# Kernel optimization log

Measured on AMD Instinct MI355X. Metric: run time of the kernel, lower is better.

## Reference

```python
import jax, jax.numpy as jnp
import numpy as np

V, E, H, T = 50000, 128, 256, 9
H2 = H // 2
B, S = 128, 512


def setup_inputs() -> dict:
    key = jax.random.key(0)
    ks = jax.random.split(key, 12)
    sc = 0.05
    return {
        "x": jax.random.randint(ks[0], (B, S), 0, V, dtype=jnp.int64) if False else jax.random.randint(ks[0], (B, S), 0, V).astype(jnp.int64),
        "mask": jnp.ones((B, S), dtype=jnp.int32),
        "embed": jax.random.normal(ks[1], (V, E), jnp.float32) * sc,
        "W_ih_f": jax.random.normal(ks[2], (4 * H2, E), jnp.float32) * sc,
        "W_hh_f": jax.random.normal(ks[3], (4 * H2, H2), jnp.float32) * sc,
        "b_f": jax.random.normal(ks[4], (4 * H2,), jnp.float32) * sc,
        "W_ih_b": jax.random.normal(ks[5], (4 * H2, E), jnp.float32) * sc,
        "W_hh_b": jax.random.normal(ks[6], (4 * H2, H2), jnp.float32) * sc,
        "b_b": jax.random.normal(ks[7], (4 * H2,), jnp.float32) * sc,
        "W_out": jax.random.normal(ks[8], (T, H), jnp.float32) * sc,
        "b_out": jax.random.normal(ks[9], (T,), jnp.float32) * sc,
        "start_trans": jax.random.normal(ks[10], (T,), jnp.float32) * sc,
        "trans": jax.random.normal(ks[11], (T, T), jnp.float32) * sc,
        "end_trans": jax.random.normal(jax.random.fold_in(key, 99), (T,), jnp.float32) * sc,
    }


def _lstm_dir(xg, W_hh, reverse):
    # xg: [B,S,4*H2] precomputed input projections (+bias)
    if reverse:
        xg = xg[:, ::-1]
    b = xg.shape[0]
    h0 = jnp.zeros((b, H2), xg.dtype)

    def step(carry, xt):
        h, c = carry
        g = xt + h @ W_hh.T
        i, f, gg, o = jnp.split(g, 4, axis=-1)
        c = jax.nn.sigmoid(f) * c + jax.nn.sigmoid(i) * jnp.tanh(gg)
        h = jax.nn.sigmoid(o) * jnp.tanh(c)
        return (h, c), h

    _, hs = jax.lax.scan(step, (h0, h0), jnp.swapaxes(xg, 0, 1))
    hs = jnp.swapaxes(hs, 0, 1)  # [B,S,H2]
    if reverse:
        hs = hs[:, ::-1]
    return hs


def _emissions(x, embed, W_ih_f, W_hh_f, b_f, W_ih_b, W_hh_b, b_b, W_out, b_out):
    emb = embed[x]  # [B,S,E]
    xg_f = jnp.einsum('bse,ge->bsg', emb, W_ih_f) + b_f
    xg_b = jnp.einsum('bse,ge->bsg', emb, W_ih_b) + b_b
    h_f = _lstm_dir(xg_f, W_hh_f, False)
    h_b = _lstm_dir(xg_b, W_hh_b, True)
    feats = jnp.concatenate([h_f, h_b], axis=-1)  # [B,S,H]
    return jnp.einsum('bsh,th->bst', feats, W_out) + b_out  # [B,S,T]


def _viterbi(emissions, mask, start_trans, trans, end_trans):
    # emissions [B,S,T], mask [B,S] (1 = valid prefix)
    m = mask.astype(bool)
    score0 = start_trans + emissions[:, 0]  # [B,T]

    def fwd_step(score, inp):
        em_t, m_t = inp  # [B,T], [B]
        nxt = score[:, :, None] + trans[None] + em_t[:, None, :]  # [B,prev,next]
        best = nxt.max(axis=1)
        idx = nxt.argmax(axis=1).astype(jnp.int32)  # [B,T] backpointers
        score = jnp.where(m_t[:, None], best, score)
        return score, idx

    em_rest = jnp.swapaxes(emissions[:, 1:], 0, 1)  # [S-1,B,T]
    m_rest = jnp.swapaxes(m[:, 1:], 0, 1)  # [S-1,B]
    score, history = jax.lax.scan(fwd_step, score0, (em_rest, m_rest))
    final = score + end_trans
    best_scores = final.max(axis=-1)  # [B]
    cur = final.argmax(axis=-1).astype(jnp.int32)  # [B] tag at last valid step

    def back_step(cur, inp):
        hist_t, m_t = inp  # [B,T], [B]
        tag = jnp.where(m_t, cur, -1)  # -1 pads positions beyond seq end
        prev = jnp.take_along_axis(hist_t, cur[:, None], axis=1)[:, 0]
        cur = jnp.where(m_t, prev, cur)
        return cur, tag

    cur0, tags_rev = jax.lax.scan(back_step, cur, (history[::-1], m_rest[::-1]))
    paths = jnp.concatenate(
        [cur0[:, None], jnp.swapaxes(tags_rev, 0, 1)[:, ::-1]], axis=1)  # [B,S]
    return paths, best_scores


def reference(x, mask, embed, W_ih_f, W_hh_f, b_f, W_ih_b, W_hh_b, b_b,
              W_out, b_out, start_trans, trans, end_trans):
    emissions = _emissions(x, embed, W_ih_f, W_hh_f, b_f,
                           W_ih_b, W_hh_b, b_b, W_out, b_out)
    paths, best_scores = _viterbi(emissions, mask, start_trans, trans, end_trans)
    return paths, best_scores
```

## Files before the change

kernel.cpp:

```cpp
#include <hip/hip_runtime.h>
#include <stdint.h>

#define S_LEN 512
#define NT 9

typedef __attribute__((ext_vector_type(8)))  short          bf16x8;
typedef __attribute__((ext_vector_type(4)))  float          f32x4;
typedef __attribute__((ext_vector_type(16))) unsigned short u16x16;
typedef __attribute__((ext_vector_type(4)))  unsigned int   u32x4;

static __device__ __forceinline__ unsigned short f2bf(float f) {
    union { float f; unsigned u; } c; c.f = f;
    return (unsigned short)((c.u + 0x7fffu + ((c.u >> 16) & 1u)) >> 16);
}
static __device__ __forceinline__ float bf2f(unsigned short h) {
    union { unsigned u; float f; } c; c.u = ((unsigned)h) << 16;
    return c.f;
}
static __device__ __forceinline__ bf16x8 cvt8(const float* p) {
    f32x4 a = *(const f32x4*)p, b = *(const f32x4*)(p + 4);
    bf16x8 fr;
    fr[0]=(short)f2bf(a[0]); fr[1]=(short)f2bf(a[1]); fr[2]=(short)f2bf(a[2]); fr[3]=(short)f2bf(a[3]);
    fr[4]=(short)f2bf(b[0]); fr[5]=(short)f2bf(b[1]); fr[6]=(short)f2bf(b[2]); fr[7]=(short)f2bf(b[3]);
    return fr;
}
static __device__ __forceinline__ float sigf(float x) {
    return __builtin_amdgcn_rcpf(1.0f + __expf(-x));
}
static __device__ __forceinline__ float tanhf_(float x) {
    return 1.0f - 2.0f * __builtin_amdgcn_rcpf(1.0f + __expf(2.0f * x));
}
static __device__ __forceinline__ float sel4(f32x4 a, int l4) {
    float x01 = (l4 & 1) ? a[1] : a[0];
    float x23 = (l4 & 1) ? a[3] : a[2];
    return (l4 & 2) ? x23 : x01;
}

static __device__ __forceinline__ void wg_barrier_lds() {
    asm volatile("s_waitcnt lgkmcnt(0)" ::: "memory");
    __builtin_amdgcn_s_barrier();
    asm volatile("" ::: "memory");
}

__global__ __launch_bounds__(512) void k_xg(
    const int* __restrict__ x, const float* __restrict__ embed,
    const float* __restrict__ Wf, const float* __restrict__ bF,
    const float* __restrict__ Wb, const float* __restrict__ bB,
    unsigned short* __restrict__ xg)
{
    const int dir = blockIdx.y, s = blockIdx.x;
    const float* __restrict__ W    = dir ? Wb : Wf;
    const float* __restrict__ bias = dir ? bB : bF;
    const int tid = threadIdx.x;
    const int wv = tid >> 6, L = tid & 63, l15 = L & 15, l4 = L >> 4;

    bf16x8 Bf[4][4];
    float  bq[4];
#pragma unroll
    for (int q = 0; q < 4; ++q) {
        const int gate = q * 128 + wv * 16 + l15;
        bq[q] = bias[gate];
#pragma unroll
        for (int kt = 0; kt < 4; ++kt)
            Bf[q][kt] = cvt8(W + gate * 128 + kt * 32 + l4 * 8);
    }

    __shared__ int tokL[128];
    __shared__ unsigned short stage[2048];

    if (tid < 128) tokL[tid] = x[tid * S_LEN + s];
    const int srow = tid >> 5, scol = tid & 31;
    __syncthreads();

    f32x4 v0 = *(const f32x4*)(embed + (size_t)tokL[srow]      * 128 + scol * 4);
    f32x4 v1 = *(const f32x4*)(embed + (size_t)tokL[16 + srow] * 128 + scol * 4);

    for (int bt16 = 0; bt16 < 8; ++bt16) {
        wg_barrier_lds();
        {
            unsigned short b4[4];
            b4[0]=f2bf(v0[0]); b4[1]=f2bf(v0[1]); b4[2]=f2bf(v0[2]); b4[3]=f2bf(v0[3]);
            int byte = srow * 256 + ((scol * 8) ^ ((srow & 7) << 4));
            *(uint2*)((char*)stage + byte) = *(const uint2*)b4;
        }
        wg_barrier_lds();
        const int nt2 = (bt16 < 6) ? (bt16 + 2) : bt16;
        f32x4 v2 = *(const f32x4*)(embed + (size_t)tokL[nt2 * 16 + srow] * 128 + scol * 4);

        bf16x8 A[4];
#pragma unroll
        for (int kt = 0; kt < 4; ++kt) {
            int byte = l15 * 256 + ((kt * 64 + l4 * 16) ^ ((l15 & 7) << 4));
            A[kt] = *(const bf16x8*)((const char*)stage + byte);
        }
        unsigned short ov[16];
#pragma unroll
        for (int q = 0; q < 4; ++q) {
            f32x4 acc = { bq[q], bq[q], bq[q], bq[q] };
#pragma unroll
            for (int kt = 0; kt < 4; ++kt)
                acc = __builtin_amdgcn_mfma_f32_16x16x32_bf16(A[kt], Bf[q][kt], acc, 0, 0, 0);
            ov[q*4+0]=f2bf(acc[0]); ov[q*4+1]=f2bf(acc[1]);
            ov[q*4+2]=f2bf(acc[2]); ov[q*4+3]=f2bf(acc[3]);
        }
        unsigned short* dst = xg +
            (((((size_t)s * 2 + dir) * 32 + bt16 * 4 + l4) * 8 + wv) * 256 + l15 * 16);
        *(u32x4*)dst       = *(const u32x4*)&ov[0];
        *(u32x4*)(dst + 8) = *(const u32x4*)&ov[8];
        v0 = v1; v1 = v2;
    }
}

__global__ __launch_bounds__(512) void k_lstm(
    const unsigned short* __restrict__ xg,
    const float* __restrict__ Whf, const float* __restrict__ Whb,
    unsigned short* __restrict__ feats)
{
    const int dir = blockIdx.y, bt = blockIdx.x;
    const float* __restrict__ Wh = dir ? Whb : Whf;
    const int tid = threadIdx.x, w = tid >> 6, L = tid & 63, l15 = L & 15, l4 = L >> 4;

    bf16x8 Bf[4][4];
#pragma unroll
    for (int q = 0; q < 4; ++q)
#pragma unroll
        for (int kt = 0; kt < 4; ++kt)
            Bf[q][kt] = cvt8(Wh + (q * 128 + w * 16 + l15) * 128 + kt * 32 + l4 * 8);

    __shared__ unsigned short hl[2048];
    for (int i = tid; i < 1024; i += 512) ((unsigned*)hl)[i] = 0;

    const int ar = l15 & 3;
    int rdoff[4];
#pragma unroll
    for (int kt = 0; kt < 4; ++kt) {
        int p = (kt * 4 + l4 + 2 * ar) & 15;
        rdoff[kt] = ar * 256 + p * 16;
    }
    const int hc = w * 16 + l15;
    const int wroff = l4 * 256 + (((hc >> 3) + 2 * l4) & 15) * 16 + (hc & 7) * 2;

    float c = 0.f;
    const size_t xstep = (size_t)2 * 32 * 8 * 256;
    const size_t xbase = (((size_t)dir * 32 + bt) * 8 + w) * 256 + l15 * 16;
    unsigned short* fptr = feats + ((size_t)(bt * 4 + l4) * 512) * 256 + dir * 128 + hc;

    u16x16 x0 = *(const u16x16*)(xg + xbase + (size_t)(dir ? 511 : 0) * xstep);
    u16x16 x1 = *(const u16x16*)(xg + xbase + (size_t)(dir ? 510 : 1) * xstep);
    __syncthreads();

    for (int t = 0; t < 512; ++t) {
        const char* bufR = (const char*)hl + (t & 1) * 1024;
        char*       bufW = (char*)hl + ((t & 1) ^ 1) * 1024;

        const int tc = (t < 510) ? (t + 2) : t;
        const int s2 = dir ? (511 - tc) : tc;
        u16x16 x2 = *(const u16x16*)(xg + xbase + (size_t)s2 * xstep);

        bf16x8 A[4];
#pragma unroll
        for (int kt = 0; kt < 4; ++kt)
            A[kt] = *(const bf16x8*)(bufR + rdoff[kt]);

        f32x4 acc[4];
#pragma unroll
        for (int q = 0; q < 4; ++q) {
            f32x4 a0 = { bf2f(x0[q*4+0]), bf2f(x0[q*4+1]), bf2f(x0[q*4+2]), bf2f(x0[q*4+3]) };
#pragma unroll
            for (int kt = 0; kt < 4; ++kt)
                a0 = __builtin_amdgcn_mfma_f32_16x16x32_bf16(A[kt], Bf[q][kt], a0, 0, 0, 0);
            acc[q] = a0;
        }
        float ig = sigf(sel4(acc[0], l4));
        float fg = sigf(sel4(acc[1], l4));
        float gg = tanhf_(sel4(acc[2], l4));
        float og = sigf(sel4(acc[3], l4));
        c = fg * c + ig * gg;
        float h = og * tanhf_(c);
        unsigned short hb = f2bf(h);
        *(unsigned short*)(bufW + wroff) = hb;
        const int s_pos = dir ? (511 - t) : t;
        fptr[(size_t)s_pos * 256] = hb;
        wg_barrier_lds();
        x0 = x1; x1 = x2;
    }
}

__global__ __launch_bounds__(256) void k_emis(
    const unsigned short* __restrict__ feats,
    const float* __restrict__ Wout, float* __restrict__ emp)
{
    const int tid = threadIdx.x;
    const int wid = blockIdx.x * 4 + (tid >> 6);
    const int L = tid & 63, l15 = L & 15, l4 = L >> 4;
    const int b = wid >> 5, sg = wid & 31;

    bf16x8 Of[2][4];
#pragma unroll
    for (int d = 0; d < 2; ++d)
#pragma unroll
        for (int kt = 0; kt < 4; ++kt) { bf16x8 z;
#pragma unroll
            for (int i = 0; i < 8; ++i) z[i] = 0; Of[d][kt] = z; }
    if (l15 < NT) {
#pragma unroll
        for (int d = 0; d < 2; ++d)
#pragma unroll
            for (int kt = 0; kt < 4; ++kt)
                Of[d][kt] = cvt8(Wout + l15 * 256 + d * 128 + kt * 32 + l4 * 8);
    }

    const unsigned short* frow = feats + ((size_t)b * 512 + sg * 16 + l15) * 256;
#pragma unroll
    for (int d = 0; d < 2; ++d) {
        bf16x8 A[4];
#pragma unroll
        for (int kt = 0; kt < 4; ++kt)
            A[kt] = *(const bf16x8*)(frow + d * 128 + kt * 32 + l4 * 8);
        f32x4 em0 = {0, 0, 0, 0};
#pragma unroll
        for (int kt = 0; kt < 4; ++kt)
            em0 = __builtin_amdgcn_mfma_f32_16x16x32_bf16(A[kt], Of[d][kt], em0, 0, 0, 0);
        if (l15 < NT) {
#pragma unroll
            for (int j = 0; j < 4; ++j)
                emp[((size_t)(d * 128 + b) * 512 + sg * 16 + l4 * 4 + j) * 9 + l15] = em0[j];
        }
    }
}

__global__ __launch_bounds__(256) void k_viterbi(
    const float* __restrict__ emp, const int* __restrict__ mask,
    const float* __restrict__ bout, const float* __restrict__ startt,
    const float* __restrict__ trans, const float* __restrict__ endt,
    float* __restrict__ out)
{
    const int b = blockIdx.x, tid = threadIdx.x;
    __shared__ float em[512 * 9];
    __shared__ int   msk[512];
    __shared__ unsigned char hist[512 * 9];
    __shared__ unsigned char Gl[32 * 12];
    __shared__ unsigned char bound[32];
    __shared__ int curS;

    const float* pf = emp + (size_t)b * 4608;
    const float* pb = emp + (size_t)(128 + b) * 4608;
    for (int i = tid; i < 4608; i += 256) {
        unsigned q = ((unsigned)i * 7282u) >> 16;
        em[i] = pf[i] + pb[i] + bout[i - 9 * q];
    }
    for (int i = tid; i < 512; i += 256) msk[i] = mask[b * 512 + i];
    __syncthreads();

    if (tid < 64) {
        const int k = (tid < NT) ? tid : 0;
        float trk[9];
#pragma unroll
        for (int j = 0; j < NT; ++j) trk[j] = trans[j * 9 + k];
        float score = startt[k] + em[k];
        for (int t = 1; t < 512; ++t) {
            float v[9];
#pragma unroll
            for (int j = 0; j < NT; ++j) v[j] = __shfl(score, j, 64) + trk[j];
            float m01 = fmaxf(v[0], v[1]), m23 = fmaxf(v[2], v[3]);
            float m45 = fmaxf(v[4], v[5]), m67 = fmaxf(v[6], v[7]);
            float m = fmaxf(fmaxf(fmaxf(m01, m23), fmaxf(m45, m67)), v[8]);
            int bi = 0;
#pragma unroll
            for (int j = 8; j >= 0; --j) if (v[j] == m) bi = j;
            if (msk[t]) score = m + em[t * 9 + k];
            if (tid < NT) hist[t * 9 + tid] = (unsigned char)bi;
        }
        float fin = score + endt[k];
        float bs = -3e38f; int cur = 0;
#pragma unroll
        for (int j = 0; j < NT; ++j) {
            float vv = __shfl(fin, j, 64);
            if (vv > bs) { bs = vv; cur = j; }
        }
        if (tid == 0) { curS = cur; out[65536 + b] = bs; }
    }
    __syncthreads();

    if (tid < 32) {
        const int m = tid;
        int G[9];
#pragma unroll
        for (int k = 0; k < NT; ++k) G[k] = k;
        const int hi = (m == 31) ? 511 : (16 * m + 16);
        for (int t = hi; t >= 16 * m + 1; --t) {
            if (msk[t]) {
#pragma unroll
                for (int k = 0; k < NT; ++k) G[k] = hist[t * 9 + G[k]];
            }
        }
#pragma unroll
        for (int k = 0; k < NT; ++k) Gl[m * 12 + k] = (unsigned char)G[k];
    }
    __syncthreads();

    if (tid == 0) {
        int e = curS;
        bound[31] = (unsigned char)e;
        for (int m = 31; m >= 1; --m) { e = Gl[m * 12 + e]; bound[m - 1] = (unsigned char)e; }
        out[(size_t)b * 512] = (float)Gl[0 * 12 + e];
    }
    __syncthreads();

    if (tid < 32) {
        const int m = tid;
        int ccur = bound[m];
        const int hi = (m == 31) ? 511 : (16 * m + 16);
        for (int t = hi; t >= 16 * m + 1; --t) {
            const int mt = msk[t];
            out[(size_t)b * 512 + t] = (float)(mt ? ccur : -1);
            if (mt) ccur = hist[t * 9 + ccur];
        }
    }
}

extern "C" void kernel_launch(void* const* d_in, const int* in_sizes, int n_in,
                              void* d_out, int out_size, void* d_ws, size_t ws_size,
                              hipStream_t stream) {
    const int*   x      = (const int*)d_in[0];
    const int*   mask   = (const int*)d_in[1];
    const float* embed  = (const float*)d_in[2];
    const float* Wihf   = (const float*)d_in[3];
    const float* Whhf   = (const float*)d_in[4];
    const float* bf_    = (const float*)d_in[5];
    const float* Wihb   = (const float*)d_in[6];
    const float* Whhb   = (const float*)d_in[7];
    const float* bb_    = (const float*)d_in[8];
    const float* Wout   = (const float*)d_in[9];
    const float* bout   = (const float*)d_in[10];
    const float* startt = (const float*)d_in[11];
    const float* trans  = (const float*)d_in[12];
    const float* endt   = (const float*)d_in[13];

    unsigned short* xg    = (unsigned short*)d_ws;
    float*          emp   = (float*)((char*)d_ws + (size_t)134217728);
    unsigned short* feats = (unsigned short*)((char*)d_ws + (size_t)138936320);
    float*          out   = (float*)d_out;

    k_xg     <<<dim3(512, 2), 512, 0, stream>>>(x, embed, Wihf, bf_, Wihb, bb_, xg);
    k_lstm   <<<dim3(32, 2),  512, 0, stream>>>(xg, Whhf, Whhb, feats);
    k_emis   <<<1024,         256, 0, stream>>>(feats, Wout, emp);
    k_viterbi<<<128,          256, 0, stream>>>(emp, mask, bout, startt, trans, endt, out);
}
```

Measured before the change: 462.7 us.

## Repack xg so each LSTM lane loads only its four gate values

The xg projection output is re-laid out so each lane of the recurrent kernel reads just the four gate pre-activations it needs (one u16x4) rather than a 16-element vector. The A-operand row mapping changes (ar = l15>>2) so the useful MFMA output sits in element 0, which removes the per-lane select. The time loop is unrolled by two with a macro, and the feats pointer is advanced incrementally. This cuts global loads and register pressure on the serial critical path, at the cost of narrower, more scattered stores in k_xg.

```diff
diff --git a/kernel.cpp b/kernel.cpp
--- a/kernel.cpp
+++ b/kernel.cpp
@@ -6,7 +6,7 @@
 
 typedef __attribute__((ext_vector_type(8)))  short          bf16x8;
 typedef __attribute__((ext_vector_type(4)))  float          f32x4;
-typedef __attribute__((ext_vector_type(16))) unsigned short u16x16;
+typedef __attribute__((ext_vector_type(4)))  unsigned short u16x4;
 typedef __attribute__((ext_vector_type(4)))  unsigned int   u32x4;
 
 static __device__ __forceinline__ unsigned short f2bf(float f) {
@@ -29,11 +29,6 @@
 }
 static __device__ __forceinline__ float tanhf_(float x) {
     return 1.0f - 2.0f * __builtin_amdgcn_rcpf(1.0f + __expf(2.0f * x));
-}
-static __device__ __forceinline__ float sel4(f32x4 a, int l4) {
-    float x01 = (l4 & 1) ? a[1] : a[0];
-    float x23 = (l4 & 1) ? a[3] : a[2];
-    return (l4 & 2) ? x23 : x01;
 }
 
 static __device__ __forceinline__ void wg_barrier_lds() {
@@ -75,6 +70,8 @@
     f32x4 v0 = *(const f32x4*)(embed + (size_t)tokL[srow]      * 128 + scol * 4);
     f32x4 v1 = *(const f32x4*)(embed + (size_t)tokL[16 + srow] * 128 + scol * 4);
 
+    const int hc = wv * 16 + l15;
+
     for (int bt16 = 0; bt16 < 8; ++bt16) {
         wg_barrier_lds();
         {
@@ -93,20 +90,24 @@
             int byte = l15 * 256 + ((kt * 64 + l4 * 16) ^ ((l15 & 7) << 4));
             A[kt] = *(const bf16x8*)((const char*)stage + byte);
         }
-        unsigned short ov[16];
+        f32x4 acc[4];
 #pragma unroll
         for (int q = 0; q < 4; ++q) {
-            f32x4 acc = { bq[q], bq[q], bq[q], bq[q] };
+            f32x4 a0 = { bq[q], bq[q], bq[q], bq[q] };
 #pragma unroll
             for (int kt = 0; kt < 4; ++kt)
-                acc = __builtin_amdgcn_mfma_f32_16x16x32_bf16(A[kt], Bf[q][kt], acc, 0, 0, 0);
-            ov[q*4+0]=f2bf(acc[0]); ov[q*4+1]=f2bf(acc[1]);
-            ov[q*4+2]=f2bf(acc[2]); ov[q*4+3]=f2bf(acc[3]);
-        }
-        unsigned short* dst = xg +
-            (((((size_t)s * 2 + dir) * 32 + bt16 * 4 + l4) * 8 + wv) * 256 + l15 * 16);
-        *(u32x4*)dst       = *(const u32x4*)&ov[0];
-        *(u32x4*)(dst + 8) = *(const u32x4*)&ov[8];
+                a0 = __builtin_amdgcn_mfma_f32_16x16x32_bf16(A[kt], Bf[q][kt], a0, 0, 0, 0);
+            acc[q] = a0;
+        }
+#pragma unroll
+        for (int j = 0; j < 4; ++j) {
+            u16x4 sv;
+#pragma unroll
+            for (int q = 0; q < 4; ++q) sv[q] = f2bf(acc[q][j]);
+            unsigned short* dst = xg +
+                (((size_t)s * 2 + dir) * 128 + bt16 * 16 + l4 * 4 + j) * 512 + hc * 4;
+            *(u16x4*)dst = sv;
+        }
         v0 = v1; v1 = v2;
     }
 }
@@ -130,7 +131,7 @@
     __shared__ unsigned short hl[2048];
     for (int i = tid; i < 1024; i += 512) ((unsigned*)hl)[i] = 0;
 
-    const int ar = l15 & 3;
+    const int ar = l15 >> 2;
     int rdoff[4];
 #pragma unroll
     for (int kt = 0; kt < 4; ++kt) {
@@ -141,49 +142,59 @@
     const int wroff = l4 * 256 + (((hc >> 3) + 2 * l4) & 15) * 16 + (hc & 7) * 2;
 
     float c = 0.f;
-    const size_t xstep = (size_t)2 * 32 * 8 * 256;
-    const size_t xbase = (((size_t)dir * 32 + bt) * 8 + w) * 256 + l15 * 16;
-    unsigned short* fptr = feats + ((size_t)(bt * 4 + l4) * 512) * 256 + dir * 128 + hc;
-
-    u16x16 x0 = *(const u16x16*)(xg + xbase + (size_t)(dir ? 511 : 0) * xstep);
-    u16x16 x1 = *(const u16x16*)(xg + xbase + (size_t)(dir ? 510 : 1) * xstep);
-    __syncthreads();
-
-    for (int t = 0; t < 512; ++t) {
-        const char* bufR = (const char*)hl + (t & 1) * 1024;
-        char*       bufW = (char*)hl + ((t & 1) ^ 1) * 1024;
-
-        const int tc = (t < 510) ? (t + 2) : t;
-        const int s2 = dir ? (511 - tc) : tc;
-        u16x16 x2 = *(const u16x16*)(xg + xbase + (size_t)s2 * xstep);
-
-        bf16x8 A[4];
-#pragma unroll
-        for (int kt = 0; kt < 4; ++kt)
-            A[kt] = *(const bf16x8*)(bufR + rdoff[kt]);
-
-        f32x4 acc[4];
-#pragma unroll
-        for (int q = 0; q < 4; ++q) {
-            f32x4 a0 = { bf2f(x0[q*4+0]), bf2f(x0[q*4+1]), bf2f(x0[q*4+2]), bf2f(x0[q*4+3]) };
-#pragma unroll
-            for (int kt = 0; kt < 4; ++kt)
-                a0 = __builtin_amdgcn_mfma_f32_16x16x32_bf16(A[kt], Bf[q][kt], a0, 0, 0, 0);
-            acc[q] = a0;
-        }
-        float ig = sigf(sel4(acc[0], l4));
-        float fg = sigf(sel4(acc[1], l4));
-        float gg = tanhf_(sel4(acc[2], l4));
-        float og = sigf(sel4(acc[3], l4));
-        c = fg * c + ig * gg;
-        float h = og * tanhf_(c);
-        unsigned short hb = f2bf(h);
-        *(unsigned short*)(bufW + wroff) = hb;
-        const int s_pos = dir ? (511 - t) : t;
-        fptr[(size_t)s_pos * 256] = hb;
-        wg_barrier_lds();
-        x0 = x1; x1 = x2;
-    }
+    const size_t xoff = ((size_t)(bt * 4 + l4)) * 512 + hc * 4;
+    const unsigned short* xp = xg + xoff + (size_t)dir * 65536;
+    unsigned short* fcur = feats + ((size_t)(bt * 4 + l4) * 512 + (dir ? 511 : 0)) * 256
+                                 + dir * 128 + hc;
+    const ptrdiff_t fstep = dir ? -256 : 256;
+
+    u16x4 xvA = *(const u16x4*)(xp + (size_t)(dir ? 511 : 0) * 131072);
+    u16x4 xvB = *(const u16x4*)(xp + (size_t)(dir ? 510 : 1) * 131072);
+
+    f32x4 acc[4];
+#pragma unroll
+    for (int q = 0; q < 4; ++q) acc[q] = f32x4{0.f, 0.f, 0.f, 0.f};
+
+    __syncthreads();
+
+#define LSTM_STEP(T, XV)                                                        \
+    {                                                                           \
+        const int t_ = (T);                                                     \
+        const char* bufR = (const char*)hl + (t_ & 1) * 1024;                   \
+        char*       bufW = (char*)hl + ((t_ & 1) ^ 1) * 1024;                   \
+        const int tc_ = (t_ < 510) ? (t_ + 2) : t_;                             \
+        const int s2_ = dir ? (511 - tc_) : tc_;                                \
+        u16x4 xnew = *(const u16x4*)(xp + (size_t)s2_ * 131072);                \
+        bf16x8 A_[4];                                                           \
+        _Pragma("unroll")                                                       \
+        for (int kt = 0; kt < 4; ++kt)                                          \
+            A_[kt] = *(const bf16x8*)(bufR + rdoff[kt]);                        \
+        _Pragma("unroll")                                                       \
+        for (int q = 0; q < 4; ++q) {                                           \
+            acc[q][0] = bf2f(XV[q]);                                            \
+            _Pragma("unroll")                                                   \
+            for (int kt = 0; kt < 4; ++kt)                                      \
+                acc[q] = __builtin_amdgcn_mfma_f32_16x16x32_bf16(               \
+                             A_[kt], Bf[q][kt], acc[q], 0, 0, 0);               \
+        }                                                                       \
+        float ig = sigf(acc[0][0]);                                             \
+        float fg = sigf(acc[1][0]);                                             \
+        float gg = tanhf_(acc[2][0]);                                           \
+        float og = sigf(acc[3][0]);                                             \
+        c = fg * c + ig * gg;                                                   \
+        float h_ = og * tanhf_(c);                                              \
+        unsigned short hb = f2bf(h_);                                           \
+        *(unsigned short*)(bufW + wroff) = hb;                                  \
+        *fcur = hb; fcur += fstep;                                              \
+        wg_barrier_lds();                                                       \
+        XV = xnew;                                                              \
+    }
+
+    for (int it = 0; it < 256; ++it) {
+        LSTM_STEP(2 * it,     xvA)
+        LSTM_STEP(2 * it + 1, xvB)
+    }
+#undef LSTM_STEP
 }
 
 __global__ __launch_bounds__(256) void k_emis(
```

Result: faster. 407.6 us (-11.9%).
